# Kernel optimization log

Measured on AMD Instinct MI355X. Metric: run time of the kernel, lower is better.

Reference implementation:

```python
import jax, jax.numpy as jnp
import numpy as np


def _lstm_step(h, c, x, W_ih, W_hh, b_ih, b_hh):
    # PyTorch gate order: i, f, g, o
    gates = x @ W_ih.T + b_ih + h @ W_hh.T + b_hh
    i, f, g, o = jnp.split(gates, 4, axis=-1)
    c = jax.nn.sigmoid(f) * c + jax.nn.sigmoid(i) * jnp.tanh(g)
    h = jax.nn.sigmoid(o) * jnp.tanh(c)
    return h, c


def setup_inputs() -> dict:
    key = jax.random.key(0)
    ks = jax.random.split(key, 12)
    B, T = 256, 256
    S, A, H, K = 64, 16, 512, 512
    D = S + A  # 80
    s = 1.0 / np.sqrt(H)
    u = lambda k, shape, sc: jax.random.uniform(k, shape, jnp.float32, -sc, sc)
    return {
        "traj": jax.random.normal(ks[0], (B, T, D), jnp.float32),
        "seq_len": T,
        "enc_W_ih": u(ks[1], (4 * H, D), s),
        "enc_W_hh": u(ks[2], (4 * H, H), s),
        "enc_b_ih": u(ks[3], (4 * H,), s),
        "enc_b_hh": u(ks[4], (4 * H,), s),
        "embeddings": jax.random.uniform(ks[5], (K, H), jnp.float32, -1.0 / K, 1.0 / K),
        "dec_W_ih": u(ks[6], (4 * H, D), s),
        "dec_W_hh": u(ks[7], (4 * H, H), s),
        "dec_b_ih": u(ks[8], (4 * H,), s),
        "dec_b_hh": u(ks[9], (4 * H,), s),
        "fc_W": u(ks[10], (D, H), s),
        "fc_b": u(ks[11], (D,), s),
    }


def reference(traj, seq_len, enc_W_ih, enc_W_hh, enc_b_ih, enc_b_hh,
              embeddings, dec_W_ih, dec_W_hh, dec_b_ih, dec_b_hh, fc_W, fc_b):
    B = traj.shape[0]
    H = enc_W_hh.shape[1]
    D = traj.shape[-1]

    # ---- Encoder: many-to-one LSTM, keep final hidden state ----
    def enc_step(carry, x_t):
        h, c = carry
        h, c = _lstm_step(h, c, x_t, enc_W_ih, enc_W_hh, enc_b_ih, enc_b_hh)
        return (h, c), None
    h0 = jnp.zeros((B, H), traj.dtype)
    (z, _), _ = jax.lax.scan(enc_step, (h0, h0), jnp.swapaxes(traj, 0, 1))

    # ---- Vector quantizer ----
    d = (jnp.sum(z * z, axis=1, keepdims=True)
         + jnp.sum(embeddings * embeddings, axis=1)
         - 2.0 * z @ embeddings.T)  # [B, K]
    idx = jnp.argmin(d, axis=1)
    quantized = embeddings[idx]  # [B, H]
    e_latent = jnp.mean((jax.lax.stop_gradient(quantized) - z) ** 2)
    q_latent = jnp.mean((quantized - jax.lax.stop_gradient(z)) ** 2)
    vq_loss = q_latent + 0.25 * e_latent

    def dec_step(carry, _):
        h, c, x = carry
        h, c = _lstm_step(h, c, x, dec_W_ih, dec_W_hh, dec_b_ih, dec_b_hh)
        y = h @ fc_W.T + fc_b
        return (h, c, y), y
    x0 = jnp.zeros((B, D), traj.dtype)
    c0 = jnp.zeros((B, H), traj.dtype)
    _, ys = jax.lax.scan(dec_step, (quantized, c0, x0), None, length=seq_len)
    recon = jnp.swapaxes(ys, 0, 1)  # [B, seq_len, D]
    return recon, vq_loss, idx[:, None]
```

## Files before the change

kernel.cpp:

```cpp
#include <hip/hip_runtime.h>
#include <math.h>

#define BB 256
#define TT 256
#define DDIM 80
#define HDIM 512
#define ROWSTRIDE 20480

#define WS_HA    0
#define WS_CD    131072
#define WS_BAR   262144
#define WS_HB    263168
#define WS_QUANT 394240
#define WS_VQP   525312
#define WS_BENC  525568
#define WS_BDEC0 527616
#define WS_BEFF  529664
#define WS_WEFF  531712

typedef _Float16 f16;
typedef f16 half4_t __attribute__((ext_vector_type(4)));
typedef f16 half8_t __attribute__((ext_vector_type(8)));
typedef float float4_t __attribute__((ext_vector_type(4)));

__device__ __forceinline__ float sigmoidf_(float v) { return 1.0f / (1.0f + expf(-v)); }

__device__ __forceinline__ void llc_store_f32(float* p, float v) {
  asm volatile("global_store_dword %0, %1, off sc0 sc1" :: "v"(p), "v"(v) : "memory");
}
__device__ __forceinline__ void llc_store_i32(int* p, int v) {
  asm volatile("global_store_dword %0, %1, off sc0 sc1" :: "v"(p), "v"(v) : "memory");
}
__device__ __forceinline__ int llc_load_i32(const int* p) {
  int v;
  asm volatile("global_load_dword %0, %1, off sc0 sc1\n\ts_waitcnt vmcnt(0)"
               : "=v"(v) : "v"(p) : "memory");
  return v;
}
__device__ __forceinline__ void wait_vm0() {
  asm volatile("s_waitcnt vmcnt(0)" ::: "memory");
}
__device__ __forceinline__ void llc_load_4xf4_cols(
    const float4* base,
    float4& a0, float4& a1, float4& a2, float4& a3) {
  asm volatile(
      "global_load_dwordx4 %0, %4, off sc0 sc1\n\t"
      "global_load_dwordx4 %1, %5, off sc0 sc1\n\t"
      "global_load_dwordx4 %2, %6, off sc0 sc1\n\t"
      "global_load_dwordx4 %3, %7, off sc0 sc1\n\t"
      "s_waitcnt vmcnt(0)"
      : "=&v"(a0), "=&v"(a1), "=&v"(a2), "=&v"(a3)
      : "v"(base), "v"(base + 32), "v"(base + 64), "v"(base + 96)
      : "memory");
}

__global__ __launch_bounds__(256) void zero_kernel(float4* __restrict__ p, int n4) {
  int i = blockIdx.x * 256 + threadIdx.x;
  if (i < n4) p[i] = make_float4(0.f, 0.f, 0.f, 0.f);
}

__global__ __launch_bounds__(256) void bias_init_kernel(
    const float* __restrict__ eb1, const float* __restrict__ eb2,
    const float* __restrict__ db1, const float* __restrict__ db2,
    const float* __restrict__ dWih, const float* __restrict__ fcb,
    float* __restrict__ b_enc, float* __restrict__ b_dec0,
    float* __restrict__ b_eff) {
  int n = blockIdx.x * 256 + threadIdx.x;
  b_enc[n] = eb1[n] + eb2[n];
  float bd = db1[n] + db2[n];
  b_dec0[n] = bd;
  float acc = bd;
  #pragma unroll 16
  for (int d = 0; d < DDIM; d++) acc += dWih[n * DDIM + d] * fcb[d];
  b_eff[n] = acc;
}

__global__ __launch_bounds__(256) void fold_kernel(
    const float* __restrict__ dWih, const float* __restrict__ dWhh,
    const float* __restrict__ fcW, float* __restrict__ W_eff) {
  int n = blockIdx.x;
  int tid = threadIdx.x;
  __shared__ float sw[DDIM];
  if (tid < DDIM) sw[tid] = dWih[n * DDIM + tid];
  __syncthreads();
  for (int k = tid; k < HDIM; k += 256) {
    float acc = dWhh[n * HDIM + k];
    #pragma unroll 16
    for (int d = 0; d < DDIM; d++) acc += sw[d] * fcW[d * HDIM + k];
    W_eff[n * HDIM + k] = acc;
  }
}

__global__ __launch_bounds__(256) void lstm_step_kernel(
    const float* __restrict__ Whh, const float* __restrict__ bias,
    const float* __restrict__ h_in, float* __restrict__ c,
    float* __restrict__ h_out) {
  __shared__ float sh[16][516];
  int tid = threadIdx.x;
  int rt = blockIdx.x & 15, jt = blockIdx.x >> 4;
  int row0 = rt << 4;
  for (int i = tid; i < 2048; i += 256) {
    int r = i >> 7, kq = i & 127;
    float4 v = *(const float4*)(h_in + (size_t)(row0 + r) * HDIM + (kq << 2));
    *(float4*)&sh[r][kq << 2] = v;
  }
  __syncthreads();
  int r = tid & 15, j0 = tid >> 4;
  int j = (jt << 4) + j0;
  float a0 = bias[j], a1 = bias[512 + j], a2 = bias[1024 + j], a3 = bias[1536 + j];
  const float4* w0 = (const float4*)(Whh + (size_t)j * HDIM);
  const float4* w1 = (const float4*)(Whh + (size_t)(512 + j) * HDIM);
  const float4* w2 = (const float4*)(Whh + (size_t)(1024 + j) * HDIM);
  const float4* w3 = (const float4*)(Whh + (size_t)(1536 + j) * HDIM);
  const float4* hv = (const float4*)&sh[r][0];
  #pragma unroll 4
  for (int kq = 0; kq < 128; kq++) {
    float4 h4 = hv[kq];
    float4 q0 = w0[kq], q1 = w1[kq], q2 = w2[kq], q3 = w3[kq];
    a0 += h4.x * q0.x + h4.y * q0.y + h4.z * q0.z + h4.w * q0.w;
    a1 += h4.x * q1.x + h4.y * q1.y + h4.z * q1.z + h4.w * q1.w;
    a2 += h4.x * q2.x + h4.y * q2.y + h4.z * q2.z + h4.w * q2.w;
    a3 += h4.x * q3.x + h4.y * q3.y + h4.z * q3.z + h4.w * q3.w;
  }
  size_t idx = (size_t)(row0 + r) * HDIM + j;
  float cv = c[idx];
  float cn = sigmoidf_(a1) * cv + sigmoidf_(a0) * tanhf(a2);
  float hn = sigmoidf_(a3) * tanhf(cn);
  c[idx] = cn;
  h_out[idx] = hn;
}

template <int IS_DEC>
__global__ __launch_bounds__(512, 2) void lstm_persist(
    const float* __restrict__ W,
    const float* __restrict__ Wih,
    const float* __restrict__ bias,
    const float* __restrict__ traj,
    const float* __restrict__ c_init,
    const float* __restrict__ fcW, const float* __restrict__ fcb,
    float* __restrict__ recon,
    float* __restrict__ hA, float* __restrict__ hB,
    int* __restrict__ flags) {
  constexpr int KT  = IS_DEC ? 16 : 19;
  constexpr int AST = IS_DEC ? 520 : 616;
  constexpr int RST = 132;
  __shared__ f16 Ahi[16 * AST];
  __shared__ f16 Alo[16 * AST];
  __shared__ float red[16 * RST];
  __shared__ float ypart[IS_DEC ? 8 * 260 : 4];

  const int tid = threadIdx.x;
  const int bid = blockIdx.x;
  const int rt = bid & 15, jt = bid >> 4;
  const int r0 = rt * 16, d0 = jt * 32;
  const int wv = __builtin_amdgcn_readfirstlane(tid >> 6);
  const int l15 = tid & 15;
  const int q = (tid >> 4) & 3;
  const int dh = wv >> 2, nt = wv & 3;

  #define SPLITC(vv, k) { \
    int off = (tid >> 5) * AST + (((tid & 31) + (k) * 32) << 2); \
    half4_t hi4, lo4; \
    float f0 = vv.x, f1 = vv.y, f2 = vv.z, f3 = vv.w; \
    f16 a = (f16)f0, b = (f16)f1, cc = (f16)f2, d = (f16)f3; \
    hi4[0] = a; hi4[1] = b; hi4[2] = cc; hi4[3] = d; \
    lo4[0] = (f16)(f0 - (float)a); lo4[1] = (f16)(f1 - (float)b); \
    lo4[2] = (f16)(f2 - (float)cc); lo4[3] = (f16)(f3 - (float)d); \
    *(half4_t*)&Ahi[off] = hi4; *(half4_t*)&Alo[off] = lo4; }

  const int grow = nt * 512 + d0 + dh * 16 + l15;
  half8_t Whi[KT], Wlo[KT];
  #pragma unroll
  for (int kt = 0; kt < KT; kt++) {
    #pragma unroll
    for (int j = 0; j < 8; j++) {
      int k = kt * 32 + q * 8 + j;
      float w;
      if (k < 512) w = W[(size_t)grow * HDIM + k];
      else {
        int kx = k - 512;
        w = (!IS_DEC && kx < DDIM) ? Wih[(size_t)grow * DDIM + kx] : 0.f;
      }
      f16 hi = (f16)w;
      Whi[kt][j] = hi;
      Wlo[kt][j] = (f16)(w - (float)hi);
    }
  }
  const float breg = bias[grow];

  half8_t Fhi[2], Flo[2];
  float ybias = 0.f;
  if (IS_DEC && jt < 5) {
    const int drow = jt * 16 + l15;
    #pragma unroll
    for (int kk = 0; kk < 2; kk++) {
      const int kt = wv * 2 + kk;
      #pragma unroll
      for (int j = 0; j < 8; j++) {
        float w = fcW[(size_t)drow * HDIM + kt * 32 + q * 8 + j];
        f16 hi = (f16)w;
        Fhi[kk][j] = hi;
        Flo[kk][j] = (f16)(w - (float)hi);
      }
    }
    ybias = fcb[jt * 16 + l15];
  }

  const int eb = tid >> 5, ed = tid & 31;
  float c_reg = IS_DEC ? c_init[(size_t)(r0 + eb) * HDIM + d0 + ed] : 0.f;
  __syncthreads();

  #define MFMA_RANGE(LO, HI) { \
    _Pragma("unroll") \
    for (int kt = (LO); kt < (HI); kt++) { \
      half8_t ahi = *(const half8_t*)&Ahi[abase + kt * 32]; \
      half8_t alo = *(const half8_t*)&Alo[abase + kt * 32]; \
      if (kt & 1) { \
        acc1 = __builtin_amdgcn_mfma_f32_16x16x32_f16(ahi, Whi[kt], acc1, 0, 0, 0); \
        acc1 = __builtin_amdgcn_mfma_f32_16x16x32_f16(alo, Whi[kt], acc1, 0, 0, 0); \
        acc1 = __builtin_amdgcn_mfma_f32_16x16x32_f16(ahi, Wlo[kt], acc1, 0, 0, 0); \
        acc1 = __builtin_amdgcn_mfma_f32_16x16x32_f16(alo, Wlo[kt], acc1, 0, 0, 0); \
      } else { \
        acc0 = __builtin_amdgcn_mfma_f32_16x16x32_f16(ahi, Whi[kt], acc0, 0, 0, 0); \
        acc0 = __builtin_amdgcn_mfma_f32_16x16x32_f16(alo, Whi[kt], acc0, 0, 0, 0); \
        acc0 = __builtin_amdgcn_mfma_f32_16x16x32_f16(ahi, Wlo[kt], acc0, 0, 0, 0); \
        acc0 = __builtin_amdgcn_mfma_f32_16x16x32_f16(alo, Wlo[kt], acc0, 0, 0, 0); \
      } \
    } }

  const int t_begin = IS_DEC ? 1 : 0;
  for (int t = t_begin; t < TT; t++) {
    const float* hin = (t & 1) ? hB : hA;
    float* hout = (t & 1) ? hA : hB;

    float4 xv0;
    if (!IS_DEC && tid < 384) {
      int row = tid / 24, c4 = tid % 24;
      xv0 = (c4 < 20)
          ? *(const float4*)(traj + (size_t)(r0 + row) * ROWSTRIDE +
                             (size_t)t * DDIM + c4 * 4)
          : make_float4(0.f, 0.f, 0.f, 0.f);
    }

    float4 v0, v1, v2, v3;
    const float4* base =
        (const float4*)(hin + (size_t)r0 * HDIM) + (tid >> 5) * 128 + (tid & 31);
    const bool is_t0 = (!IS_DEC && t == 0);
    if (!is_t0) {
      asm volatile(
          "global_load_dwordx4 %0, %4, off sc0 sc1\n\t"
          "global_load_dwordx4 %1, %5, off sc0 sc1\n\t"
          "global_load_dwordx4 %2, %6, off sc0 sc1\n\t"
          "global_load_dwordx4 %3, %7, off sc0 sc1"
          : "=&v"(v0), "=&v"(v1), "=&v"(v2), "=&v"(v3)
          : "v"(base), "v"(base + 32), "v"(base + 64), "v"(base + 96)
          : "memory");
      asm volatile("s_waitcnt vmcnt(2)" ::: "memory");
      __builtin_amdgcn_sched_barrier(0);
      SPLITC(v0, 0); SPLITC(v1, 1);
    } else {
      const int fo = (tid >> 5) * AST + ((tid & 31) << 4);
      uint4 z4; z4.x = 0; z4.y = 0; z4.z = 0; z4.w = 0;
      *(uint4*)&Ahi[fo] = z4; *(uint4*)&Ahi[fo + 8] = z4;
      *(uint4*)&Alo[fo] = z4; *(uint4*)&Alo[fo + 8] = z4;
    }
    __syncthreads();

    float4_t acc0 = {breg, breg, breg, breg};
    float4_t acc1 = {0.f, 0.f, 0.f, 0.f};
    const int abase = l15 * AST + q * 8;
    MFMA_RANGE(0, 8);

    if (!is_t0) {
      asm volatile("s_waitcnt vmcnt(0)" ::: "memory");
      __builtin_amdgcn_sched_barrier(0);
      SPLITC(v2, 2); SPLITC(v3, 3);
    }
    if (!IS_DEC && tid < 384) {
      int row = tid / 24, c4 = tid % 24;
      int off = row * AST + 512 + c4 * 4;
      half4_t hi4, lo4;
      float f0 = xv0.x, f1 = xv0.y, f2 = xv0.z, f3 = xv0.w;
      f16 a = (f16)f0, b = (f16)f1, cc = (f16)f2, d = (f16)f3;
      hi4[0] = a; hi4[1] = b; hi4[2] = cc; hi4[3] = d;
      lo4[0] = (f16)(f0 - (float)a); lo4[1] = (f16)(f1 - (float)b);
      lo4[2] = (f16)(f2 - (float)cc); lo4[3] = (f16)(f3 - (float)d);
      *(half4_t*)&Ahi[off] = hi4; *(half4_t*)&Alo[off] = lo4;
    }
    __syncthreads();
    MFMA_RANGE(8, KT);
    {
      float4_t C = acc0 + acc1;
      #pragma unroll
      for (int i = 0; i < 4; i++)
        red[(q * 4 + i) * RST + nt * 32 + dh * 16 + l15] = C[i];
    }
    __syncthreads();

    {
      float ig = red[eb * RST + ed];
      float fg = red[eb * RST + 32 + ed];
      float gg = red[eb * RST + 64 + ed];
      float og = red[eb * RST + 96 + ed];
      float cn = sigmoidf_(fg) * c_reg + sigmoidf_(ig) * tanhf(gg);
      c_reg = cn;
      llc_store_f32(&hout[(size_t)(r0 + eb) * HDIM + d0 + ed],
                    sigmoidf_(og) * tanhf(cn));
    }
    wait_vm0();
    __syncthreads();

    const int done = t - t_begin + 1;
    const bool do_bar = IS_DEC || t < TT - 1;
    if (do_bar && tid == 0) llc_store_i32(&flags[rt * 16 + jt], done);

    if (IS_DEC && jt < 5) {
      float4_t ya = {0.f, 0.f, 0.f, 0.f};
      #pragma unroll
      for (int kk = 0; kk < 2; kk++) {
        const int kt = wv * 2 + kk;
        const int ao = l15 * AST + kt * 32 + q * 8;
        half8_t ahi = *(const half8_t*)&Ahi[ao];
        half8_t alo = *(const half8_t*)&Alo[ao];
        ya = __builtin_amdgcn_mfma_f32_16x16x32_f16(ahi, Fhi[kk], ya, 0, 0, 0);
        ya = __builtin_amdgcn_mfma_f32_16x16x32_f16(alo, Fhi[kk], ya, 0, 0, 0);
        ya = __builtin_amdgcn_mfma_f32_16x16x32_f16(ahi, Flo[kk], ya, 0, 0, 0);
        ya = __builtin_amdgcn_mfma_f32_16x16x32_f16(alo, Flo[kk], ya, 0, 0, 0);
      }
      #pragma unroll
      for (int i = 0; i < 4; i++)
        ypart[wv * 260 + (q * 4 + i) * 16 + l15] = ya[i];
    }
    if (IS_DEC) __syncthreads();
    if (IS_DEC && jt < 5 && tid < 256) {
      float acc = ybias;
      #pragma unroll
      for (int w8 = 0; w8 < 8; w8++) acc += ypart[w8 * 260 + tid];
      recon[(size_t)(r0 + (tid >> 4)) * ROWSTRIDE + (size_t)(t - 1) * DDIM +
            jt * 16 + (tid & 15)] = acc;
    }

    if (do_bar) {
      if (tid < 64) {
        const int* fp = flags + rt * 16 + (tid & 15);
        while (llc_load_i32(fp) < done) {}
      }
      __syncthreads();
    }
  }

  if (IS_DEC) {
    if (jt >= 5) return;
    {
      const float4* base =
          (const float4*)(hA + (size_t)r0 * HDIM) + (tid >> 5) * 128 + (tid & 31);
      float4 v0, v1, v2, v3;
      llc_load_4xf4_cols(base, v0, v1, v2, v3);
      SPLITC(v0, 0); SPLITC(v1, 1); SPLITC(v2, 2); SPLITC(v3, 3);
    }
    __syncthreads();
    {
      float4_t ya = {0.f, 0.f, 0.f, 0.f};
      #pragma unroll
      for (int kk = 0; kk < 2; kk++) {
        const int kt = wv * 2 + kk;
        const int ao = l15 * AST + kt * 32 + q * 8;
        half8_t ahi = *(const half8_t*)&Ahi[ao];
        half8_t alo = *(const half8_t*)&Alo[ao];
        ya = __builtin_amdgcn_mfma_f32_16x16x32_f16(ahi, Fhi[kk], ya, 0, 0, 0);
        ya = __builtin_amdgcn_mfma_f32_16x16x32_f16(alo, Fhi[kk], ya, 0, 0, 0);
        ya = __builtin_amdgcn_mfma_f32_16x16x32_f16(ahi, Flo[kk], ya, 0, 0, 0);
        ya = __builtin_amdgcn_mfma_f32_16x16x32_f16(alo, Flo[kk], ya, 0, 0, 0);
      }
      #pragma unroll
      for (int i = 0; i < 4; i++)
        ypart[wv * 260 + (q * 4 + i) * 16 + l15] = ya[i];
    }
    __syncthreads();
    if (tid < 256) {
      float acc = ybias;
      #pragma unroll
      for (int w8 = 0; w8 < 8; w8++) acc += ypart[w8 * 260 + tid];
      recon[(size_t)(r0 + (tid >> 4)) * ROWSTRIDE + (size_t)255 * DDIM +
            jt * 16 + (tid & 15)] = acc;
    }
  }
  #undef SPLITC
  #undef MFMA_RANGE
}

__global__ __launch_bounds__(256) void vq_kernel(
    const float* __restrict__ z, const float* __restrict__ emb,
    float* __restrict__ quant, float* __restrict__ vq_part,
    float* __restrict__ out_idx) {
  __shared__ float sz[512];
  __shared__ float sd[256];
  __shared__ int si[256];
  int b = blockIdx.x, tid = threadIdx.x;
  sz[tid] = z[(size_t)b * HDIM + tid];
  sz[tid + 256] = z[(size_t)b * HDIM + 256 + tid];
  __syncthreads();
  float bd = 3.4e38f;
  int bk = 0;
  for (int k = tid; k < 512; k += 256) {
    const float4* e4 = (const float4*)(emb + (size_t)k * HDIM);
    const float4* z4 = (const float4*)sz;
    float dot = 0.f, ee = 0.f;
    #pragma unroll 4
    for (int qq = 0; qq < 128; qq++) {
      float4 ev = e4[qq], zv = z4[qq];
      dot += ev.x * zv.x + ev.y * zv.y + ev.z * zv.z + ev.w * zv.w;
      ee += ev.x * ev.x + ev.y * ev.y + ev.z * ev.z + ev.w * ev.w;
    }
    float dist = ee - 2.f * dot;
    if (dist < bd) { bd = dist; bk = k; }
  }
  sd[tid] = bd; si[tid] = bk;
  __syncthreads();
  for (int s = 128; s > 0; s >>= 1) {
    if (tid < s) {
      float od = sd[tid + s]; int ok = si[tid + s];
      if (od < sd[tid] || (od == sd[tid] && ok < si[tid])) { sd[tid] = od; si[tid] = ok; }
    }
    __syncthreads();
  }
  int kbest = si[0];
  __syncthreads();
  float e0 = emb[(size_t)kbest * HDIM + tid];
  float e1 = emb[(size_t)kbest * HDIM + 256 + tid];
  quant[(size_t)b * HDIM + tid] = e0;
  quant[(size_t)b * HDIM + 256 + tid] = e1;
  float q0 = e0 - sz[tid], q1 = e1 - sz[tid + 256];
  sd[tid] = q0 * q0 + q1 * q1;
  __syncthreads();
  for (int st = 128; st > 0; st >>= 1) {
    if (tid < st) sd[tid] += sd[tid + st];
    __syncthreads();
  }
  if (tid == 0) { vq_part[b] = sd[0]; out_idx[b] = (float)kbest; }
}

__global__ __launch_bounds__(256) void vq_reduce_kernel(const float* __restrict__ vq_part,
                                                        float* __restrict__ out_loss) {
  __shared__ float s[256];
  int tid = threadIdx.x;
  s[tid] = vq_part[tid];
  __syncthreads();
  for (int st = 128; st > 0; st >>= 1) {
    if (tid < st) s[tid] += s[tid + st];
    __syncthreads();
  }
  if (tid == 0) out_loss[0] = s[0] * 1.25f / (float)(BB * HDIM);
}

extern "C" void kernel_launch(void* const* d_in, const int* in_sizes, int n_in,
                              void* d_out, int out_size, void* d_ws, size_t ws_size,
                              hipStream_t stream) {
  const float* traj = (const float*)d_in[0];
  const float* eWih = (const float*)d_in[2];
  const float* eWhh = (const float*)d_in[3];
  const float* eb1  = (const float*)d_in[4];
  const float* eb2  = (const float*)d_in[5];
  const float* emb  = (const float*)d_in[6];
  const float* dWih = (const float*)d_in[7];
  const float* dWhh = (const float*)d_in[8];
  const float* db1  = (const float*)d_in[9];
  const float* db2  = (const float*)d_in[10];
  const float* fcW  = (const float*)d_in[11];
  const float* fcb  = (const float*)d_in[12];

  float* out = (float*)d_out;
  float* recon = out;
  float* out_loss = out + 5242880;
  float* out_idx = out + 5242881;

  float* ws = (float*)d_ws;
  float* hA      = ws + WS_HA;
  float* cD      = ws + WS_CD;
  int*   bar     = (int*)(ws + WS_BAR);
  float* hB      = ws + WS_HB;
  float* quant   = ws + WS_QUANT;
  float* vq_part = ws + WS_VQP;
  float* b_enc   = ws + WS_BENC;
  float* b_dec0  = ws + WS_BDEC0;
  float* b_eff   = ws + WS_BEFF;
  float* W_eff   = ws + WS_WEFF;

  zero_kernel<<<257, 256, 0, stream>>>((float4*)ws, 65792);
  bias_init_kernel<<<8, 256, 0, stream>>>(eb1, eb2, db1, db2, dWih, fcb,
                                          b_enc, b_dec0, b_eff);
  fold_kernel<<<2048, 256, 0, stream>>>(dWih, dWhh, fcW, W_eff);

  lstm_persist<0><<<256, 512, 0, stream>>>(
      eWhh, eWih, b_enc, traj, nullptr, nullptr, nullptr, nullptr, hA, hB, bar);

  vq_kernel<<<256, 256, 0, stream>>>(hA, emb, quant, vq_part, out_idx);
  vq_reduce_kernel<<<1, 256, 0, stream>>>(vq_part, out_loss);

  lstm_step_kernel<<<512, 256, 0, stream>>>(dWhh, b_dec0, quant, cD, hB);
  lstm_persist<1><<<256, 512, 0, stream>>>(
      W_eff, nullptr, b_eff, nullptr, cD, fcW, fcb, recon, hA, hB, bar + 256);
}
```

Measured before the change: 2.131 ms.

## Use fast sigmoid/tanh intrinsics, pipeline flag polling, and skip decoder barrier for idle blocks

Replaces expf/tanhf-based sigmoid and tanh with exp2 and reciprocal hardware intrinsics, which shortens the gate-activation step on the serial critical path of each timestep. The inter-block barrier poll now keeps four flag loads in flight instead of one blocking load, with the aim of cutting spin-wait latency. The decoder's fc reduction syncthreads moves inside the jt<5 branch, so blocks that do not produce recon outputs skip one barrier. The fast activations lose some accuracy, and the branch-local __syncthreads is only safe because jt is uniform across the block.

New measurement: 1.973 ms. 7.4% less time.

```diff
diff --git a/kernel.cpp b/kernel.cpp
--- a/kernel.cpp
+++ b/kernel.cpp
@@ -23,7 +23,12 @@
 typedef f16 half8_t __attribute__((ext_vector_type(8)));
 typedef float float4_t __attribute__((ext_vector_type(4)));
 
-__device__ __forceinline__ float sigmoidf_(float v) { return 1.0f / (1.0f + expf(-v)); }
+__device__ __forceinline__ float sigmoid_fast(float v) {
+  return __builtin_amdgcn_rcpf(1.0f + __builtin_amdgcn_exp2f(-1.44269504f * v));
+}
+__device__ __forceinline__ float tanh_fast(float v) {
+  return 2.0f * __builtin_amdgcn_rcpf(1.0f + __builtin_amdgcn_exp2f(-2.88539008f * v)) - 1.0f;
+}
 
 __device__ __forceinline__ void llc_store_f32(float* p, float v) {
   asm volatile("global_store_dword %0, %1, off sc0 sc1" :: "v"(p), "v"(v) : "memory");
@@ -31,15 +36,40 @@
 __device__ __forceinline__ void llc_store_i32(int* p, int v) {
   asm volatile("global_store_dword %0, %1, off sc0 sc1" :: "v"(p), "v"(v) : "memory");
 }
-__device__ __forceinline__ int llc_load_i32(const int* p) {
-  int v;
-  asm volatile("global_load_dword %0, %1, off sc0 sc1\n\ts_waitcnt vmcnt(0)"
-               : "=v"(v) : "v"(p) : "memory");
-  return v;
-}
 __device__ __forceinline__ void wait_vm0() {
   asm volatile("s_waitcnt vmcnt(0)" ::: "memory");
 }
+
+__device__ __forceinline__ void poll_flag4(const int* fp, int done) {
+  int a0, a1, a2, a3;
+  asm volatile(
+      "global_load_dword %0, %4, off sc0 sc1\n\t"
+      "global_load_dword %1, %4, off sc0 sc1\n\t"
+      "global_load_dword %2, %4, off sc0 sc1\n\t"
+      "Lpoll%=:\n\t"
+      "global_load_dword %3, %4, off sc0 sc1\n\t"
+      "s_waitcnt vmcnt(3)\n\t"
+      "v_cmp_gt_i32 vcc, %5, %0\n\t"
+      "s_cbranch_vccz Ldone%=\n\t"
+      "global_load_dword %0, %4, off sc0 sc1\n\t"
+      "s_waitcnt vmcnt(3)\n\t"
+      "v_cmp_gt_i32 vcc, %5, %1\n\t"
+      "s_cbranch_vccz Ldone%=\n\t"
+      "global_load_dword %1, %4, off sc0 sc1\n\t"
+      "s_waitcnt vmcnt(3)\n\t"
+      "v_cmp_gt_i32 vcc, %5, %2\n\t"
+      "s_cbranch_vccz Ldone%=\n\t"
+      "global_load_dword %2, %4, off sc0 sc1\n\t"
+      "s_waitcnt vmcnt(3)\n\t"
+      "v_cmp_gt_i32 vcc, %5, %3\n\t"
+      "s_cbranch_vccnz Lpoll%=\n\t"
+      "Ldone%=:\n\t"
+      "s_waitcnt vmcnt(0)"
+      : "=&v"(a0), "=&v"(a1), "=&v"(a2), "=&v"(a3)
+      : "v"(fp), "s"(done)
+      : "vcc", "memory");
+}
+
 __device__ __forceinline__ void llc_load_4xf4_cols(
     const float4* base,
     float4& a0, float4& a1, float4& a2, float4& a3) {
@@ -124,8 +154,8 @@
   }
   size_t idx = (size_t)(row0 + r) * HDIM + j;
   float cv = c[idx];
-  float cn = sigmoidf_(a1) * cv + sigmoidf_(a0) * tanhf(a2);
-  float hn = sigmoidf_(a3) * tanhf(cn);
+  float cn = sigmoid_fast(a1) * cv + sigmoid_fast(a0) * tanh_fast(a2);
+  float hn = sigmoid_fast(a3) * tanh_fast(cn);
   c[idx] = cn;
   h_out[idx] = hn;
 }
@@ -302,10 +332,10 @@
       float fg = red[eb * RST + 32 + ed];
       float gg = red[eb * RST + 64 + ed];
       float og = red[eb * RST + 96 + ed];
-      float cn = sigmoidf_(fg) * c_reg + sigmoidf_(ig) * tanhf(gg);
+      float cn = sigmoid_fast(fg) * c_reg + sigmoid_fast(ig) * tanh_fast(gg);
       c_reg = cn;
       llc_store_f32(&hout[(size_t)(r0 + eb) * HDIM + d0 + ed],
-                    sigmoidf_(og) * tanhf(cn));
+                    sigmoid_fast(og) * tanh_fast(cn));
     }
     wait_vm0();
     __syncthreads();
@@ -330,21 +360,18 @@
       #pragma unroll
       for (int i = 0; i < 4; i++)
         ypart[wv * 260 + (q * 4 + i) * 16 + l15] = ya[i];
-    }
-    if (IS_DEC) __syncthreads();
-    if (IS_DEC && jt < 5 && tid < 256) {
-      float acc = ybias;
-      #pragma unroll
-      for (int w8 = 0; w8 < 8; w8++) acc += ypart[w8 * 260 + tid];
-      recon[(size_t)(r0 + (tid >> 4)) * ROWSTRIDE + (size_t)(t - 1) * DDIM +
-            jt * 16 + (tid & 15)] = acc;
+      __syncthreads();
+      if (tid < 256) {
+        float acc = ybias;
+        #pragma unroll
+        for (int w8 = 0; w8 < 8; w8++) acc += ypart[w8 * 260 + tid];
+        recon[(size_t)(r0 + (tid >> 4)) * ROWSTRIDE + (size_t)(t - 1) * DDIM +
+              jt * 16 + (tid & 15)] = acc;
+      }
     }
 
     if (do_bar) {
-      if (tid < 64) {
-        const int* fp = flags + rt * 16 + (tid & 15);
-        while (llc_load_i32(fp) < done) {}
-      }
+      if (tid < 64) poll_flag4(flags + rt * 16 + (tid & 15), done);
       __syncthreads();
     }
   }
@@ -356,6 +383,7 @@
           (const float4*)(hA + (size_t)r0 * HDIM) + (tid >> 5) * 128 + (tid & 31);
       float4 v0, v1, v2, v3;
       llc_load_4xf4_cols(base, v0, v1, v2, v3);
+      __builtin_amdgcn_sched_barrier(0);
       SPLITC(v0, 0); SPLITC(v1, 1); SPLITC(v2, 2); SPLITC(v3, 3);
     }
     __syncthreads();
```
